# Performance work log

Measured on AMD Instinct MI355X. Metric: run time of the kernel, lower is better.

Reference implementation:

```python
import jax, jax.numpy as jnp
import numpy as np
import math

DIM = 3      # coordinate dim per node
N_NODES = 15 # 45 / 3
HEADS = 3
D_K = 1


def _spatial_graph():
    # ST-GCN style 15-joint skeleton: (self, inward, outward) adjacency, shape (3,15,15)
    edges = [(1, 0), (2, 1), (3, 2), (4, 0), (5, 4), (6, 5), (7, 0),
             (8, 7), (9, 8), (10, 9), (11, 8), (12, 11), (13, 8), (14, 13)]
    self_a = np.eye(N_NODES, dtype=np.float32)
    inward = np.zeros((N_NODES, N_NODES), dtype=np.float32)
    for i, j in edges:
        inward[i, j] = 1.0
    outward = inward.T.copy()
    return jnp.asarray(np.stack([self_a, inward, outward], axis=0))


def setup_inputs() -> dict:
    key = jax.random.key(0)
    ks = jax.random.split(key, 11)
    bs, T, F = 32, 2048, DIM * N_NODES
    bound3 = 1.0 / math.sqrt(DIM)
    bound45 = 1.0 / math.sqrt(F)
    return {
        "q": jax.random.normal(ks[0], (bs, T, F), jnp.float32),
        "k": jax.random.normal(ks[1], (bs, T, F), jnp.float32),
        "v": jax.random.normal(ks[2], (bs, T, F), jnp.float32),
        "wq": jax.random.uniform(ks[3], (DIM, DIM), jnp.float32, -bound3, bound3),
        "bq": jax.random.uniform(ks[4], (DIM,), jnp.float32, -bound3, bound3),
        "wk": jax.random.uniform(ks[5], (DIM, DIM), jnp.float32, -bound3, bound3),
        "bk": jax.random.uniform(ks[6], (DIM,), jnp.float32, -bound3, bound3),
        "wv": jax.random.uniform(ks[7], (DIM, DIM), jnp.float32, -bound3, bound3),
        "bv": jax.random.uniform(ks[8], (DIM,), jnp.float32, -bound3, bound3),
        "wo": jax.random.uniform(ks[9], (F, F), jnp.float32, -bound45, bound45),
        "bo": jax.random.uniform(ks[10], (F,), jnp.float32, -bound45, bound45),
        "graph": _spatial_graph(),
        "is_test": 0,
    }


def _project(x, w, b, bs, T):
    # (bs,T,45) -> (bs,T,3,15) -> (bs,T,15,3) -> linear -> (bs,T,15,3,1) -> (bs,T,3,15,1)
    x = x.reshape(bs, T, DIM, N_NODES).transpose(0, 1, 3, 2)
    x = x @ w.T + b
    return x.reshape(bs, T, N_NODES, HEADS, D_K).transpose(0, 1, 3, 2, 4)


def reference(q, k, v, wq, bq, wk, bk, wv, bv, wo, bo, graph, is_test):
    bs, T, F = q.shape
    qh = _project(q, wq, bq, bs, T)  # (bs,T,h,15,1)
    kh = _project(k, wk, bk, bs, T)
    vh = _project(v, wv, bv, bs, T)
    # abs scores with graph mask, shape (bs,T,h,15,15)
    scores = jnp.abs(jnp.einsum('bthnd,bthmd->bthnm', qh, kh) / math.sqrt(D_K))
    graph_tot = graph.sum(0)  # (15,15)
    scores = jnp.where(graph_tot == 0, jnp.float32(-1e9), scores)
    # softmax over flattened 15*15 grid
    att = jax.nn.softmax(scores.reshape(bs, T, HEADS, N_NODES * N_NODES), axis=-1)
    att = att.reshape(bs, T, HEADS, N_NODES, N_NODES)
    out = jnp.einsum('bthnm,bthmd->bthnd', att, vh)  # (bs,T,h,15,1)
    concat = out.transpose(0, 1, 3, 2, 4).reshape(bs, T, F)
    return concat @ wo.T + bo
```

## Files before the change

### kernel.cpp

```cpp
#include <hip/hip_runtime.h>


#define SLAB 2880

__device__ __forceinline__ void glds16(const float* g, float* l) {
  __builtin_amdgcn_global_load_lds(
      (const __attribute__((address_space(1))) void*)g,
      (__attribute__((address_space(3))) void*)l, 16, 0, 0);
}

__global__ void __launch_bounds__(256)
mha_spatial_kernel(const float* __restrict__ q, const float* __restrict__ k,
                   const float* __restrict__ v,
                   const float* __restrict__ wq, const float* __restrict__ bq,
                   const float* __restrict__ wk, const float* __restrict__ bk,
                   const float* __restrict__ wv, const float* __restrict__ bv,
                   const float* __restrict__ wo, const float* __restrict__ bo,
                   float* __restrict__ out)
{
  constexpr int MOFF[16] = {0,4,7,10,12,15,18,20,23,28,31,33,36,38,41,43};
  constexpr int MN[43] = {0,1,4,7,  0,1,2,  1,2,3,  2,3,  0,4,5,  4,5,6,
                          5,6,  0,7,8,  7,8,9,11,13,  8,9,10,  9,10,
                          8,11,12,  11,12,  8,13,14,  13,14};

  __shared__ float sm[3 * SLAB];
  const int tid = threadIdx.x;
  const int p = tid & 63;
  const int w = __builtin_amdgcn_readfirstlane(tid >> 6);
  const int h = (w < 2) ? w : 2;
  const size_t base = (size_t)blockIdx.x * SLAB;

  {
    const float* gq = q + base;
    const float* gk = k + base;
    const float* gv = v + base;
    float* l0 = sm;
    float* l1 = sm + SLAB;
    float* l2 = sm + 2 * SLAB;
#pragma unroll
    for (int i = 0; i < 3; ++i) {
      const int idx = i * 256 + tid;
      if (idx < 720) {
        const int off = idx * 4;
        glds16(gq + off, l0 + off);
        glds16(gk + off, l1 + off);
        glds16(gv + off, l2 + off);
      }
    }
  }

  const float wq0 = wq[h*3+0], wq1 = wq[h*3+1], wq2 = wq[h*3+2], bq0 = bq[h];
  const float wk0 = wk[h*3+0], wk1 = wk[h*3+1], wk2 = wk[h*3+2], bk0 = bk[h];
  const float wv0 = wv[h*3+0], wv1 = wv[h*3+1], wv2 = wv[h*3+2], bv0 = bv[h];

  __syncthreads();

  float oh[15];
  float rz;
  {
    const float* xq = sm + p * 45;
    const float* xk = sm + SLAB + p * 45;
    const float* xv = sm + 2 * SLAB + p * 45;
    float aq[15];
#pragma unroll
    for (int n = 0; n < 15; ++n) {
      aq[n] = fabsf(bq0 + xq[n] * wq0 + xq[15 + n] * wq1 + xq[30 + n] * wq2);
      oh[n] = 0.0f;
    }
    float Z0 = 0.0f, Z1 = 0.0f;
#pragma unroll
    for (int m = 0; m < 15; ++m) {
      const float akm = fabsf(bk0 + xk[m] * wk0 + xk[15 + m] * wk1 + xk[30 + m] * wk2);
      const float vvm = bv0 + xv[m] * wv0 + xv[15 + m] * wv1 + xv[30 + m] * wv2;
#pragma unroll
      for (int t = MOFF[m]; t < MOFF[m + 1]; ++t) {
        const int n = MN[t];
        const float e = __expf(aq[n] * akm);
        if (t & 1) Z1 += e; else Z0 += e;
        oh[n] += e * vvm;
      }
    }
    rz = 1.0f / (Z0 + Z1);
  }

  __syncthreads();

  {
    float* crow = sm + p * 45;
#pragma unroll
    for (int n = 0; n < 15; ++n) {
      const bool mine = (w == 0) || (w == 1) ||
                        ((w == 2) ? (n < 8) : (n >= 8));
      if (mine) crow[n * 3 + h] = oh[n] * rz;
    }
  }
  __syncthreads();

  {
    const int fbase = w * 11;
    const int NR = (w == 3) ? 12 : 11;
    const float* crow = sm + p * 45;
    float acc[12];
#pragma unroll
    for (int j = 0; j < 12; ++j)
      if (j < NR) acc[j] = bo[fbase + j];
#pragma unroll
    for (int c = 0; c < 3; ++c) {
      float cg[15];
#pragma unroll
      for (int t = 0; t < 15; ++t) cg[t] = crow[c * 15 + t];
#pragma unroll
      for (int t = 0; t < 15; ++t) {
#pragma unroll
        for (int j = 0; j < 12; ++j)
          if (j < NR)
            acc[j] = fmaf(cg[t], wo[(fbase + j) * 45 + c * 15 + t], acc[j]);
      }
    }
    float* yrow = sm + SLAB + p * 45;
#pragma unroll
    for (int j = 0; j < 12; ++j)
      if (j < NR) yrow[fbase + j] = acc[j];
  }
  __syncthreads();

  float* gout = out + base;
  const float* ysrc = sm + SLAB;
#pragma unroll
  for (int i = 0; i < 3; ++i) {
    const int idx = i * 256 + tid;
    if (idx < 720)
      *(float4*)(gout + idx * 4) = *(const float4*)(ysrc + idx * 4);
  }
}

extern "C" void kernel_launch(void* const* d_in, const int* in_sizes, int n_in,
                              void* d_out, int out_size, void* d_ws, size_t ws_size,
                              hipStream_t stream) {
  const float* q  = (const float*)d_in[0];
  const float* k  = (const float*)d_in[1];
  const float* v  = (const float*)d_in[2];
  const float* wq = (const float*)d_in[3];
  const float* bq = (const float*)d_in[4];
  const float* wk = (const float*)d_in[5];
  const float* bk = (const float*)d_in[6];
  const float* wv = (const float*)d_in[7];
  const float* bv = (const float*)d_in[8];
  const float* wo = (const float*)d_in[9];
  const float* bo = (const float*)d_in[10];
  float* out = (float*)d_out;

  hipLaunchKernelGGL(mha_spatial_kernel, dim3(1024), dim3(256), 0, stream,
                     q, k, v, wq, bq, wk, bk, wv, bv, wo, bo, out);
}
```

Baseline: 21.54 us.

## Use three waves per block and overlap V load with score computation

The block shrinks from four waves to three, one per head. This removes the duplicated head-2 wave and its split ownership of the concat writes, and gives each wave a uniform set of 15 output-projection columns. The V slab is now fetched asynchronously after the first barrier, so its transfer overlaps the exponential/score phase. The 43 exponentials are kept in registers and consumed after a barrier that covers the V load. The trade-off is higher register pressure and fewer threads issuing the initial loads.

```diff
diff --git a/kernel.cpp b/kernel.cpp
--- a/kernel.cpp
+++ b/kernel.cpp
@@ -9,7 +9,7 @@
       (__attribute__((address_space(3))) void*)l, 16, 0, 0);
 }
 
-__global__ void __launch_bounds__(256)
+__global__ void __launch_bounds__(192)
 mha_spatial_kernel(const float* __restrict__ q, const float* __restrict__ k,
                    const float* __restrict__ v,
                    const float* __restrict__ wq, const float* __restrict__ bq,
@@ -26,25 +26,21 @@
   __shared__ float sm[3 * SLAB];
   const int tid = threadIdx.x;
   const int p = tid & 63;
-  const int w = __builtin_amdgcn_readfirstlane(tid >> 6);
-  const int h = (w < 2) ? w : 2;
+  const int h = __builtin_amdgcn_readfirstlane(tid >> 6);
   const size_t base = (size_t)blockIdx.x * SLAB;
 
   {
     const float* gq = q + base;
     const float* gk = k + base;
-    const float* gv = v + base;
     float* l0 = sm;
     float* l1 = sm + SLAB;
-    float* l2 = sm + 2 * SLAB;
 #pragma unroll
-    for (int i = 0; i < 3; ++i) {
-      const int idx = i * 256 + tid;
+    for (int i = 0; i < 4; ++i) {
+      const int idx = i * 192 + tid;
       if (idx < 720) {
         const int off = idx * 4;
         glds16(gq + off, l0 + off);
         glds16(gk + off, l1 + off);
-        glds16(gv + off, l2 + off);
       }
     }
   }
@@ -55,29 +51,34 @@
 
   __syncthreads();
 
-  float oh[15];
+  {
+    const float* gv = v + base;
+    float* l2 = sm + 2 * SLAB;
+#pragma unroll
+    for (int i = 0; i < 4; ++i) {
+      const int idx = i * 192 + tid;
+      if (idx < 720) glds16(gv + idx * 4, l2 + idx * 4);
+    }
+  }
+
+  float e[43];
   float rz;
   {
     const float* xq = sm + p * 45;
     const float* xk = sm + SLAB + p * 45;
-    const float* xv = sm + 2 * SLAB + p * 45;
     float aq[15];
 #pragma unroll
-    for (int n = 0; n < 15; ++n) {
+    for (int n = 0; n < 15; ++n)
       aq[n] = fabsf(bq0 + xq[n] * wq0 + xq[15 + n] * wq1 + xq[30 + n] * wq2);
-      oh[n] = 0.0f;
-    }
     float Z0 = 0.0f, Z1 = 0.0f;
 #pragma unroll
     for (int m = 0; m < 15; ++m) {
       const float akm = fabsf(bk0 + xk[m] * wk0 + xk[15 + m] * wk1 + xk[30 + m] * wk2);
-      const float vvm = bv0 + xv[m] * wv0 + xv[15 + m] * wv1 + xv[30 + m] * wv2;
 #pragma unroll
       for (int t = MOFF[m]; t < MOFF[m + 1]; ++t) {
-        const int n = MN[t];
-        const float e = __expf(aq[n] * akm);
-        if (t & 1) Z1 += e; else Z0 += e;
-        oh[n] += e * vvm;
+        const float et = __expf(aq[MN[t]] * akm);
+        e[t] = et;
+        if (t & 1) Z1 += et; else Z0 += et;
       }
     }
     rz = 1.0f / (Z0 + Z1);
@@ -85,25 +86,34 @@
 
   __syncthreads();
 
+  float oh[15];
+  {
+    const float* xv = sm + 2 * SLAB + p * 45;
+#pragma unroll
+    for (int n = 0; n < 15; ++n) oh[n] = 0.0f;
+#pragma unroll
+    for (int m = 0; m < 15; ++m) {
+      const float vvm = bv0 + xv[m] * wv0 + xv[15 + m] * wv1 + xv[30 + m] * wv2;
+#pragma unroll
+      for (int t = MOFF[m]; t < MOFF[m + 1]; ++t)
+        oh[MN[t]] += e[t] * vvm;
+    }
+  }
+
   {
     float* crow = sm + p * 45;
 #pragma unroll
-    for (int n = 0; n < 15; ++n) {
-      const bool mine = (w == 0) || (w == 1) ||
-                        ((w == 2) ? (n < 8) : (n >= 8));
-      if (mine) crow[n * 3 + h] = oh[n] * rz;
-    }
+    for (int n = 0; n < 15; ++n)
+      crow[n * 3 + h] = oh[n] * rz;
   }
   __syncthreads();
 
   {
-    const int fbase = w * 11;
-    const int NR = (w == 3) ? 12 : 11;
+    const int fbase = h * 15;
     const float* crow = sm + p * 45;
-    float acc[12];
+    float acc[15];
 #pragma unroll
-    for (int j = 0; j < 12; ++j)
-      if (j < NR) acc[j] = bo[fbase + j];
+    for (int j = 0; j < 15; ++j) acc[j] = bo[fbase + j];
 #pragma unroll
     for (int c = 0; c < 3; ++c) {
       float cg[15];
@@ -112,23 +122,21 @@
 #pragma unroll
       for (int t = 0; t < 15; ++t) {
 #pragma unroll
-        for (int j = 0; j < 12; ++j)
-          if (j < NR)
-            acc[j] = fmaf(cg[t], wo[(fbase + j) * 45 + c * 15 + t], acc[j]);
+        for (int j = 0; j < 15; ++j)
+          acc[j] = fmaf(cg[t], wo[(fbase + j) * 45 + c * 15 + t], acc[j]);
       }
     }
     float* yrow = sm + SLAB + p * 45;
 #pragma unroll
-    for (int j = 0; j < 12; ++j)
-      if (j < NR) yrow[fbase + j] = acc[j];
+    for (int j = 0; j < 15; ++j) yrow[fbase + j] = acc[j];
   }
   __syncthreads();
 
   float* gout = out + base;
   const float* ysrc = sm + SLAB;
 #pragma unroll
-  for (int i = 0; i < 3; ++i) {
-    const int idx = i * 256 + tid;
+  for (int i = 0; i < 4; ++i) {
+    const int idx = i * 192 + tid;
     if (idx < 720)
       *(float4*)(gout + idx * 4) = *(const float4*)(ysrc + idx * 4);
   }
@@ -150,6 +158,6 @@
   const float* bo = (const float*)d_in[10];
   float* out = (float*)d_out;
 
-  hipLaunchKernelGGL(mha_spatial_kernel, dim3(1024), dim3(256), 0, stream,
+  hipLaunchKernelGGL(mha_spatial_kernel, dim3(1024), dim3(192), 0, stream,
                      q, k, v, wq, bq, wk, bk, wv, bv, wo, bo, out);
 }
```

After: 19.13 us. 1.13x faster.
